# Optimization experiments

Measured on AMD Instinct MI355X. Metric: run time of the kernel, lower is better.

Reference implementation:

```python
import jax, jax.numpy as jnp
import numpy as np

TAU = 1.0  # gumbel-softmax temperature (self.temperature)


def setup_inputs() -> dict:
    key = jax.random.key(0)
    k1, k2, k3 = jax.random.split(key, 3)
    B, N, D = 4, 1024, 64
    node_features = jax.random.normal(k1, (B, N, D), dtype=jnp.float32)
    # edge_predictor params: Linear(2D -> D), Linear(D -> 1); stored as [in, out]
    W1 = jax.random.normal(k2, (2 * D, D), dtype=jnp.float32) * (1.0 / np.sqrt(2 * D))
    b1 = jnp.zeros((D,), dtype=jnp.float32)
    W2 = jax.random.normal(k3, (D, 1), dtype=jnp.float32) * (1.0 / np.sqrt(D))
    b2 = jnp.zeros((1,), dtype=jnp.float32)
    return {"node_features": node_features, "W1": W1, "b1": b1, "W2": W2, "b2": b2}


def reference(node_features, W1, b1, W2, b2):
    B, N, D = node_features.shape
    # cat([f_i, f_j]) @ W1 == f_i @ W1[:D] + f_j @ W1[D:] -> avoid [B,N,N,2D] concat
    h_src = jnp.einsum('bnd,de->bne', node_features, W1[:D])  # [B,N,D]
    h_dst = jnp.einsum('bnd,de->bne', node_features, W1[D:])  # [B,N,D]
    hidden = jax.nn.relu(h_src[:, :, None, :] + h_dst[:, None, :, :] + b1)  # [B,N,N,D]
    edge_logits = jnp.einsum('bijd,do->bij', hidden, W2) + b2[0]  # [B,N,N]
    edge_logits = 0.5 * (edge_logits + jnp.swapaxes(edge_logits, 1, 2))
    # training branch: gumbel-softmax (hard, straight-through) over [logit, 0] pair
    paired = jnp.stack([edge_logits, jnp.zeros_like(edge_logits)], axis=-1)  # [B,N,N,2]
    g = jax.random.gumbel(jax.random.key(42), paired.shape, dtype=paired.dtype)
    y_soft = jax.nn.softmax((paired + g) / TAU, axis=-1)
    hard = jax.nn.one_hot(jnp.argmax(y_soft, axis=-1), 2, dtype=y_soft.dtype)
    y = hard + y_soft - jax.lax.stop_gradient(y_soft)  # straight-through
    adj = y[..., 0] * (1.0 - jnp.eye(N, dtype=y.dtype))
    return adj, edge_logits
```

## Files before the change

kernel.cpp:

```cpp
#include <hip/hip_runtime.h>
#include <stdint.h>
#include <math.h>

#define NB 4
#define NN 1024
#define ND 64
#define RP 68

__device__ double g_hs64[NB * NN * ND];
__device__ double g_hd64[NB * NN * ND];
__device__ float  g_hs32[NB * NN * ND];
__device__ float  g_hd32[NB * NN * ND];
__device__ double g_w2d[ND];
__device__ float  g_w2f[ND];

__device__ __forceinline__ void threefry_core(uint32_t K0, uint32_t K1,
                                              uint32_t x0, uint32_t x1,
                                              uint32_t& o0, uint32_t& o1) {
  const uint32_t K2 = K0 ^ K1 ^ 0x1BD11BDAu;
  x0 += K0; x1 += K1;
#define TF_RND(r) { x0 += x1; x1 = (x1 << r) | (x1 >> (32 - r)); x1 ^= x0; }
  TF_RND(13) TF_RND(15) TF_RND(26) TF_RND(6)
  x0 += K1; x1 += K2 + 1u;
  TF_RND(17) TF_RND(29) TF_RND(16) TF_RND(24)
  x0 += K2; x1 += K0 + 2u;
  TF_RND(13) TF_RND(15) TF_RND(26) TF_RND(6)
  x0 += K0; x1 += K1 + 3u;
  TF_RND(17) TF_RND(29) TF_RND(16) TF_RND(24)
  x0 += K1; x1 += K2 + 4u;
  TF_RND(13) TF_RND(15) TF_RND(26) TF_RND(6)
  x0 += K2; x1 += K0 + 5u;
#undef TF_RND
  o0 = x0; o1 = x1;
}

__device__ __forceinline__ uint32_t rand_word(uint32_t L) {
  uint32_t o0, o1;
  threefry_core(0u, 42u, 0u, L, o0, o1);
  return o0 ^ o1;
}

__device__ __forceinline__ float u_from_word(uint32_t w) {
  uint32_t fb = (w >> 9) | 0x3f800000u;
  float f = __uint_as_float(fb) - 1.0f;
  const float tinyf = 1.17549435e-38f;
  return fmaxf(tinyf, f + tinyf);
}

__device__ __attribute__((noinline)) float decide_fallback(int b, int i, int j,
                                                           uint32_t m, double b2d) {
  const double* hsi = g_hs64 + ((size_t)(b * NN + i)) * ND;
  const double* hdi = g_hd64 + ((size_t)(b * NN + i)) * ND;
  const double* hsj = g_hs64 + ((size_t)(b * NN + j)) * ND;
  const double* hdj = g_hd64 + ((size_t)(b * NN + j)) * ND;
  double l1 = 0.0, l2 = 0.0;
  for (int d = 0; d < ND; ++d) {
    double w = g_w2d[d];
    l1 += fmax(hsi[d] + hdj[d], 0.0) * w;
    l2 += fmax(hsj[d] + hdi[d], 0.0) * w;
  }
  double sym = 0.5 * (l1 + l2) + b2d;
  double E = exp(sym);
  double L0 = -log((double)u_from_word(rand_word(2u * m)));
  double L1 = -log((double)u_from_word(rand_word(2u * m + 1u)));
  return (E * L1 >= L0) ? 1.0f : 0.0f;
}

__global__ __launch_bounds__(256) void stage1(const float* __restrict__ nf,
                                              const float* __restrict__ W1,
                                              const float* __restrict__ b1,
                                              const float* __restrict__ W2) {
  __shared__ float w1s[2 * ND][ND];
  __shared__ float rows[4][ND];
  const int tid = threadIdx.x;
  const float4* W14 = (const float4*)W1;
  float4* w1s4 = (float4*)w1s;
  #pragma unroll
  for (int p = 0; p < 8; ++p) w1s4[tid + 256 * p] = W14[tid + 256 * p];
  const int r = tid >> 6, e = tid & 63;
  const int bn = blockIdx.x * 4 + r;
  rows[r][e] = nf[bn * ND + e];
  __syncthreads();
  double accs = 0.0, accd = 0.0;
  #pragma unroll
  for (int k = 0; k < ND; ++k) {
    double x = (double)rows[r][k];
    accs = fma(x, (double)w1s[k][e], accs);
    accd = fma(x, (double)w1s[ND + k][e], accd);
  }
  accd += (double)b1[e];
  const int o = bn * ND + e;
  g_hs64[o] = accs;  g_hd64[o] = accd;
  g_hs32[o] = (float)accs;  g_hd32[o] = (float)accd;
  if (blockIdx.x == 0 && tid < ND) {
    g_w2d[tid] = (double)W2[tid];
    g_w2f[tid] = W2[tid];
  }
}

__global__ __launch_bounds__(256, 4) void stage2(const float* __restrict__ b2,
                                                 float* __restrict__ adj,
                                                 float* __restrict__ logits) {
  const int t = blockIdx.x;
  const int b = t / 528;
  const int k = t - b * 528;
#define TRI_S(x) ((x) * 32 - ((x) * ((x) - 1)) / 2)
  int bi = (int)((65.0 - sqrt((double)(4225 - 8 * k))) * 0.5);
  while (k >= TRI_S(bi + 1)) ++bi;
  while (k < TRI_S(bi)) --bi;
  const int bj = bi + (k - TRI_S(bi));
#undef TRI_S
  const int i0 = bi * 32, j0 = bj * 32;

  __shared__ float sh_si[32][RP], sh_di[32][RP];
  __shared__ float sh_sj[32][RP], sh_dj[32][RP];
  __shared__ float w2s[ND];

  const int tid = threadIdx.x;
  {
    const float4* src_si = (const float4*)(g_hs32 + ((size_t)(b * NN + i0)) * ND);
    const float4* src_di = (const float4*)(g_hd32 + ((size_t)(b * NN + i0)) * ND);
    const float4* src_sj = (const float4*)(g_hs32 + ((size_t)(b * NN + j0)) * ND);
    const float4* src_dj = (const float4*)(g_hd32 + ((size_t)(b * NN + j0)) * ND);
    #pragma unroll
    for (int p = 0; p < 2; ++p) {
      const int q = tid + 256 * p;
      const int r = q >> 4, c4 = (q & 15) << 2;
      *(float4*)&sh_si[r][c4] = src_si[q];
      *(float4*)&sh_di[r][c4] = src_di[q];
      *(float4*)&sh_sj[r][c4] = src_sj[q];
      *(float4*)&sh_dj[r][c4] = src_dj[q];
    }
    if (tid < ND) w2s[tid] = g_w2f[tid];
  }
  __syncthreads();

  const int tx = tid & 15, ty = tid >> 4;

  float a1[2][2] = {{0.f, 0.f}, {0.f, 0.f}};
  float a2[2][2] = {{0.f, 0.f}, {0.f, 0.f}};

  #pragma unroll 4
  for (int d = 0; d < ND; d += 4) {
    float wv[4], si[2][4], di[2][4], sj[2][4], dj[2][4];
    *(float4*)wv    = *(const float4*)&w2s[d];
    *(float4*)si[0] = *(const float4*)&sh_si[ty][d];
    *(float4*)si[1] = *(const float4*)&sh_si[ty + 16][d];
    *(float4*)di[0] = *(const float4*)&sh_di[ty][d];
    *(float4*)di[1] = *(const float4*)&sh_di[ty + 16][d];
    *(float4*)sj[0] = *(const float4*)&sh_sj[tx][d];
    *(float4*)sj[1] = *(const float4*)&sh_sj[tx + 16][d];
    *(float4*)dj[0] = *(const float4*)&sh_dj[tx][d];
    *(float4*)dj[1] = *(const float4*)&sh_dj[tx + 16][d];
    #pragma unroll
    for (int dd = 0; dd < 4; ++dd) {
      const float w = wv[dd];
      #pragma unroll
      for (int a = 0; a < 2; ++a)
        #pragma unroll
        for (int c = 0; c < 2; ++c) {
          a1[a][c] = fmaf(fmaxf(si[a][dd] + dj[c][dd], 0.f), w, a1[a][c]);
          a2[a][c] = fmaf(fmaxf(sj[c][dd] + di[a][dd], 0.f), w, a2[a][c]);
        }
    }
  }

  const float b2f = b2[0];
  const double b2d = (double)b2f;

  #pragma unroll
  for (int a = 0; a < 2; ++a)
    #pragma unroll
    for (int c = 0; c < 2; ++c) {
      const int i = i0 + ty + 16 * a;
      const int j = j0 + tx + 16 * c;
      const float symf = 0.5f * (a1[a][c] + a2[a][c]) + b2f;
      const uint32_t m1 = (uint32_t)((b * NN + i) * NN + j);
      const uint32_t m2 = (uint32_t)((b * NN + j) * NN + i);

      const float E = __expf(symf);
      const float L0a = -__logf(u_from_word(rand_word(2u * m1)));
      const float L1a = -__logf(u_from_word(rand_word(2u * m1 + 1u)));
      const float L0b = -__logf(u_from_word(rand_word(2u * m2)));
      const float L1b = -__logf(u_from_word(rand_word(2u * m2 + 1u)));

      float adj1, adj2;
      if (i == j) {
        adj1 = 0.f; adj2 = 0.f;
      } else {
        const float pa = E * L1a, da = pa - L0a;
        const float pb = E * L1b, db = pb - L0b;
        const bool flagA = (fabsf(da) < 2e-3f * (pa + L0a)) || ((pa + L0a) < 2e-6f);
        const bool flagB = (fabsf(db) < 2e-3f * (pb + L0b)) || ((pb + L0b) < 2e-6f);
        adj1 = flagA ? decide_fallback(b, i, j, m1, b2d) : (da >= 0.f ? 1.f : 0.f);
        adj2 = flagB ? decide_fallback(b, i, j, m2, b2d) : (db >= 0.f ? 1.f : 0.f);
      }

      logits[m1] = symf;
      logits[m2] = symf;
      adj[m1] = adj1;
      adj[m2] = adj2;
    }
}

extern "C" void kernel_launch(void* const* d_in, const int* in_sizes, int n_in,
                              void* d_out, int out_size, void* d_ws, size_t ws_size,
                              hipStream_t stream) {
  const float* nf = (const float*)d_in[0];
  const float* W1 = (const float*)d_in[1];
  const float* b1 = (const float*)d_in[2];
  const float* W2 = (const float*)d_in[3];
  const float* b2 = (const float*)d_in[4];

  float* adj    = (float*)d_out;
  float* logits = adj + (size_t)NB * NN * NN;

  stage1<<<dim3(NB * NN / 4), dim3(256), 0, stream>>>(nf, W1, b1, W2);
  stage2<<<dim3(NB * 528), dim3(256), 0, stream>>>(b2, adj, logits);
}
```

Measured before the change: 158.8 us.

## Use packed f32 math, halve shared tiles, raise occupancy in stage2

Stage2 now stages the node-feature tiles in two 32-column halves, which cuts shared memory per block roughly in half, and raises launch bounds from 4 to 8 blocks per SIMD. The inner loop uses inline-asm v_pk_add_f32 and v_pk_fma_f32 on pairs of channels, with two partial accumulators per output that are summed at the end. The goal is higher occupancy and fewer VALU instructions for the pairwise ReLU-dot compute. In exchange it adds an extra barrier and reload phase, the per-element fmax still breaks the packing, and the reordered float summation may shift values slightly near the fallback thresholds.

```diff
diff --git a/kernel.cpp b/kernel.cpp
--- a/kernel.cpp
+++ b/kernel.cpp
@@ -5,7 +5,20 @@
 #define NB 4
 #define NN 1024
 #define ND 64
-#define RP 68
+#define RPH 36
+
+typedef float v2f __attribute__((ext_vector_type(2)));
+
+__device__ __forceinline__ v2f pk_add(v2f a, v2f b) {
+  v2f d;
+  asm("v_pk_add_f32 %0, %1, %2" : "=v"(d) : "v"(a), "v"(b));
+  return d;
+}
+__device__ __forceinline__ v2f pk_fma(v2f a, v2f b, v2f c) {
+  v2f d;
+  asm("v_pk_fma_f32 %0, %1, %2, %3" : "=v"(d) : "v"(a), "v"(b), "v"(c));
+  return d;
+}
 
 __device__ double g_hs64[NB * NN * ND];
 __device__ double g_hd64[NB * NN * ND];
@@ -98,7 +111,7 @@
   }
 }
 
-__global__ __launch_bounds__(256, 4) void stage2(const float* __restrict__ b2,
+__global__ __launch_bounds__(256, 8) void stage2(const float* __restrict__ b2,
                                                  float* __restrict__ adj,
                                                  float* __restrict__ logits) {
   const int t = blockIdx.x;
@@ -112,56 +125,75 @@
 #undef TRI_S
   const int i0 = bi * 32, j0 = bj * 32;
 
-  __shared__ float sh_si[32][RP], sh_di[32][RP];
-  __shared__ float sh_sj[32][RP], sh_dj[32][RP];
+  __shared__ float sh[4][32][RPH];
   __shared__ float w2s[ND];
 
   const int tid = threadIdx.x;
-  {
-    const float4* src_si = (const float4*)(g_hs32 + ((size_t)(b * NN + i0)) * ND);
-    const float4* src_di = (const float4*)(g_hd32 + ((size_t)(b * NN + i0)) * ND);
-    const float4* src_sj = (const float4*)(g_hs32 + ((size_t)(b * NN + j0)) * ND);
-    const float4* src_dj = (const float4*)(g_hd32 + ((size_t)(b * NN + j0)) * ND);
-    #pragma unroll
-    for (int p = 0; p < 2; ++p) {
-      const int q = tid + 256 * p;
-      const int r = q >> 4, c4 = (q & 15) << 2;
-      *(float4*)&sh_si[r][c4] = src_si[q];
-      *(float4*)&sh_di[r][c4] = src_di[q];
-      *(float4*)&sh_sj[r][c4] = src_sj[q];
-      *(float4*)&sh_dj[r][c4] = src_dj[q];
+  const int tx = tid & 15, ty = tid >> 4;
+  if (tid < ND) w2s[tid] = g_w2f[tid];
+
+  v2f a1[2][2], a2[2][2];
+  #pragma unroll
+  for (int a = 0; a < 2; ++a)
+    #pragma unroll
+    for (int c = 0; c < 2; ++c) { a1[a][c] = (v2f)(0.f); a2[a][c] = (v2f)(0.f); }
+
+  const int srow = tid >> 3;
+  const int scol = (tid & 7) << 2;
+
+  #pragma unroll
+  for (int h = 0; h < 2; ++h) {
+    if (h) __syncthreads();
+    const int d0 = h * 32;
+    #pragma unroll
+    for (int p = 0; p < 4; ++p) {
+      const float* src = (p & 1) ? g_hd32 : g_hs32;
+      const int base = (p < 2) ? i0 : j0;
+      float4 v = *(const float4*)(src + ((size_t)(b * NN + base + srow)) * ND + d0 + scol);
+      *(float4*)&sh[p][srow][scol] = v;
     }
-    if (tid < ND) w2s[tid] = g_w2f[tid];
-  }
-  __syncthreads();
-
-  const int tx = tid & 15, ty = tid >> 4;
-
-  float a1[2][2] = {{0.f, 0.f}, {0.f, 0.f}};
-  float a2[2][2] = {{0.f, 0.f}, {0.f, 0.f}};
-
-  #pragma unroll 4
-  for (int d = 0; d < ND; d += 4) {
-    float wv[4], si[2][4], di[2][4], sj[2][4], dj[2][4];
-    *(float4*)wv    = *(const float4*)&w2s[d];
-    *(float4*)si[0] = *(const float4*)&sh_si[ty][d];
-    *(float4*)si[1] = *(const float4*)&sh_si[ty + 16][d];
-    *(float4*)di[0] = *(const float4*)&sh_di[ty][d];
-    *(float4*)di[1] = *(const float4*)&sh_di[ty + 16][d];
-    *(float4*)sj[0] = *(const float4*)&sh_sj[tx][d];
-    *(float4*)sj[1] = *(const float4*)&sh_sj[tx + 16][d];
-    *(float4*)dj[0] = *(const float4*)&sh_dj[tx][d];
-    *(float4*)dj[1] = *(const float4*)&sh_dj[tx + 16][d];
-    #pragma unroll
-    for (int dd = 0; dd < 4; ++dd) {
-      const float w = wv[dd];
+    __syncthreads();
+
+    #pragma unroll
+    for (int dd = 0; dd < 32; dd += 4) {
+      const float4 w4  = *(const float4*)&w2s[d0 + dd];
+      const float4 si0 = *(const float4*)&sh[0][ty][dd];
+      const float4 si1 = *(const float4*)&sh[0][ty + 16][dd];
+      const float4 di0 = *(const float4*)&sh[1][ty][dd];
+      const float4 di1 = *(const float4*)&sh[1][ty + 16][dd];
+      const float4 sj0 = *(const float4*)&sh[2][tx][dd];
+      const float4 sj1 = *(const float4*)&sh[2][tx + 16][dd];
+      const float4 dj0 = *(const float4*)&sh[3][tx][dd];
+      const float4 dj1 = *(const float4*)&sh[3][tx + 16][dd];
+
       #pragma unroll
-      for (int a = 0; a < 2; ++a)
+      for (int k2 = 0; k2 < 2; ++k2) {
+        v2f w_, si[2], di[2], sj[2], dj[2];
+        if (k2 == 0) {
+          w_ = (v2f){w4.x, w4.y};
+          si[0] = (v2f){si0.x, si0.y}; si[1] = (v2f){si1.x, si1.y};
+          di[0] = (v2f){di0.x, di0.y}; di[1] = (v2f){di1.x, di1.y};
+          sj[0] = (v2f){sj0.x, sj0.y}; sj[1] = (v2f){sj1.x, sj1.y};
+          dj[0] = (v2f){dj0.x, dj0.y}; dj[1] = (v2f){dj1.x, dj1.y};
+        } else {
+          w_ = (v2f){w4.z, w4.w};
+          si[0] = (v2f){si0.z, si0.w}; si[1] = (v2f){si1.z, si1.w};
+          di[0] = (v2f){di0.z, di0.w}; di[1] = (v2f){di1.z, di1.w};
+          sj[0] = (v2f){sj0.z, sj0.w}; sj[1] = (v2f){sj1.z, sj1.w};
+          dj[0] = (v2f){dj0.z, dj0.w}; dj[1] = (v2f){dj1.z, dj1.w};
+        }
         #pragma unroll
-        for (int c = 0; c < 2; ++c) {
-          a1[a][c] = fmaf(fmaxf(si[a][dd] + dj[c][dd], 0.f), w, a1[a][c]);
-          a2[a][c] = fmaf(fmaxf(sj[c][dd] + di[a][dd], 0.f), w, a2[a][c]);
-        }
+        for (int a = 0; a < 2; ++a)
+          #pragma unroll
+          for (int c = 0; c < 2; ++c) {
+            v2f t1 = pk_add(si[a], dj[c]);
+            t1.x = fmaxf(t1.x, 0.f); t1.y = fmaxf(t1.y, 0.f);
+            a1[a][c] = pk_fma(t1, w_, a1[a][c]);
+            v2f t2 = pk_add(sj[c], di[a]);
+            t2.x = fmaxf(t2.x, 0.f); t2.y = fmaxf(t2.y, 0.f);
+            a2[a][c] = pk_fma(t2, w_, a2[a][c]);
+          }
+      }
     }
   }
 
@@ -174,7 +206,9 @@
     for (int c = 0; c < 2; ++c) {
       const int i = i0 + ty + 16 * a;
       const int j = j0 + tx + 16 * c;
-      const float symf = 0.5f * (a1[a][c] + a2[a][c]) + b2f;
+      const float l1 = a1[a][c].x + a1[a][c].y;
+      const float l2 = a2[a][c].x + a2[a][c].y;
+      const float symf = 0.5f * (l1 + l2) + b2f;
       const uint32_t m1 = (uint32_t)((b * NN + i) * NN + j);
       const uint32_t m2 = (uint32_t)((b * NN + j) * NN + i);
 
```

Result: slower. 171.9 us (+8.3%).

## Stage output tiles through shared memory for coalesced float4 stores and halve LDS

Applied to the files above, without the earlier changes.

Stage2 now writes logits and both adjacency tiles into shared memory, then writes them out as coalesced float4 rows for both the (i,j) and transposed (j,i) blocks. Before, each thread did scattered scalar stores, and the transposed writes had a stride of NN. The feature tiles are loaded in two 32-wide halves, which halves shared-memory use, and launch bounds go up to 8 blocks per CU for higher occupancy. RNG work is also skipped on diagonal elements. In exchange there are extra __syncthreads barriers, and the transposed reads from shared memory may hit bank conflicts.

```diff
diff --git a/kernel.cpp b/kernel.cpp
--- a/kernel.cpp
+++ b/kernel.cpp
@@ -5,7 +5,8 @@
 #define NB 4
 #define NN 1024
 #define ND 64
-#define RP 68
+#define RPH 36
+#define TS 36
 
 __device__ double g_hs64[NB * NN * ND];
 __device__ double g_hd64[NB * NN * ND];
@@ -98,7 +99,7 @@
   }
 }
 
-__global__ __launch_bounds__(256, 4) void stage2(const float* __restrict__ b2,
+__global__ __launch_bounds__(256, 8) void stage2(const float* __restrict__ b2,
                                                  float* __restrict__ adj,
                                                  float* __restrict__ logits) {
   const int t = blockIdx.x;
@@ -112,82 +113,95 @@
 #undef TRI_S
   const int i0 = bi * 32, j0 = bj * 32;
 
-  __shared__ float sh_si[32][RP], sh_di[32][RP];
-  __shared__ float sh_sj[32][RP], sh_dj[32][RP];
+  __shared__ float sh[4 * 32 * RPH];
   __shared__ float w2s[ND];
 
   const int tid = threadIdx.x;
-  {
-    const float4* src_si = (const float4*)(g_hs32 + ((size_t)(b * NN + i0)) * ND);
-    const float4* src_di = (const float4*)(g_hd32 + ((size_t)(b * NN + i0)) * ND);
-    const float4* src_sj = (const float4*)(g_hs32 + ((size_t)(b * NN + j0)) * ND);
-    const float4* src_dj = (const float4*)(g_hd32 + ((size_t)(b * NN + j0)) * ND);
-    #pragma unroll
-    for (int p = 0; p < 2; ++p) {
-      const int q = tid + 256 * p;
-      const int r = q >> 4, c4 = (q & 15) << 2;
-      *(float4*)&sh_si[r][c4] = src_si[q];
-      *(float4*)&sh_di[r][c4] = src_di[q];
-      *(float4*)&sh_sj[r][c4] = src_sj[q];
-      *(float4*)&sh_dj[r][c4] = src_dj[q];
-    }
-    if (tid < ND) w2s[tid] = g_w2f[tid];
-  }
-  __syncthreads();
-
   const int tx = tid & 15, ty = tid >> 4;
+  if (tid < ND) w2s[tid] = g_w2f[tid];
 
   float a1[2][2] = {{0.f, 0.f}, {0.f, 0.f}};
   float a2[2][2] = {{0.f, 0.f}, {0.f, 0.f}};
 
-  #pragma unroll 4
-  for (int d = 0; d < ND; d += 4) {
-    float wv[4], si[2][4], di[2][4], sj[2][4], dj[2][4];
-    *(float4*)wv    = *(const float4*)&w2s[d];
-    *(float4*)si[0] = *(const float4*)&sh_si[ty][d];
-    *(float4*)si[1] = *(const float4*)&sh_si[ty + 16][d];
-    *(float4*)di[0] = *(const float4*)&sh_di[ty][d];
-    *(float4*)di[1] = *(const float4*)&sh_di[ty + 16][d];
-    *(float4*)sj[0] = *(const float4*)&sh_sj[tx][d];
-    *(float4*)sj[1] = *(const float4*)&sh_sj[tx + 16][d];
-    *(float4*)dj[0] = *(const float4*)&sh_dj[tx][d];
-    *(float4*)dj[1] = *(const float4*)&sh_dj[tx + 16][d];
+  const int srow = tid >> 3;
+  const int scol = (tid & 7) << 2;
+
+#define SH(p, r, c) sh[((p) * 32 + (r)) * RPH + (c)]
+
+  #pragma unroll
+  for (int h = 0; h < 2; ++h) {
+    if (h) __syncthreads();
+    const int d0 = h * 32;
     #pragma unroll
-    for (int dd = 0; dd < 4; ++dd) {
-      const float w = wv[dd];
+    for (int p = 0; p < 4; ++p) {
+      const float* src = (p & 1) ? g_hd32 : g_hs32;
+      const int base = (p < 2) ? i0 : j0;
+      float4 v = *(const float4*)(src + ((size_t)(b * NN + base + srow)) * ND + d0 + scol);
+      *(float4*)&SH(p, srow, scol) = v;
+    }
+    __syncthreads();
+
+    #pragma unroll
+    for (int dd = 0; dd < 32; dd += 4) {
+      const float4 w4  = *(const float4*)&w2s[d0 + dd];
+      const float4 si0 = *(const float4*)&SH(0, ty, dd);
+      const float4 si1 = *(const float4*)&SH(0, ty + 16, dd);
+      const float4 di0 = *(const float4*)&SH(1, ty, dd);
+      const float4 di1 = *(const float4*)&SH(1, ty + 16, dd);
+      const float4 sj0 = *(const float4*)&SH(2, tx, dd);
+      const float4 sj1 = *(const float4*)&SH(2, tx + 16, dd);
+      const float4 dj0 = *(const float4*)&SH(3, tx, dd);
+      const float4 dj1 = *(const float4*)&SH(3, tx + 16, dd);
+
+      const float* wv = (const float*)&w4;
+      const float* siA[2] = {(const float*)&si0, (const float*)&si1};
+      const float* diA[2] = {(const float*)&di0, (const float*)&di1};
+      const float* sjA[2] = {(const float*)&sj0, (const float*)&sj1};
+      const float* djA[2] = {(const float*)&dj0, (const float*)&dj1};
+
       #pragma unroll
-      for (int a = 0; a < 2; ++a)
+      for (int kk = 0; kk < 4; ++kk) {
+        const float w = wv[kk];
         #pragma unroll
-        for (int c = 0; c < 2; ++c) {
-          a1[a][c] = fmaf(fmaxf(si[a][dd] + dj[c][dd], 0.f), w, a1[a][c]);
-          a2[a][c] = fmaf(fmaxf(sj[c][dd] + di[a][dd], 0.f), w, a2[a][c]);
-        }
+        for (int a = 0; a < 2; ++a)
+          #pragma unroll
+          for (int c = 0; c < 2; ++c) {
+            a1[a][c] = fmaf(fmaxf(siA[a][kk] + djA[c][kk], 0.f), w, a1[a][c]);
+            a2[a][c] = fmaf(fmaxf(sjA[c][kk] + diA[a][kk], 0.f), w, a2[a][c]);
+          }
+      }
     }
   }
 
   const float b2f = b2[0];
   const double b2d = (double)b2f;
+
+  float* Lg = sh;
+  float* A1 = sh + 32 * TS;
+  float* A2 = sh + 64 * TS;
+
+  __syncthreads();
 
   #pragma unroll
   for (int a = 0; a < 2; ++a)
     #pragma unroll
     for (int c = 0; c < 2; ++c) {
-      const int i = i0 + ty + 16 * a;
-      const int j = j0 + tx + 16 * c;
+      const int rr = ty + 16 * a;
+      const int cc = tx + 16 * c;
+      const int i = i0 + rr, j = j0 + cc;
       const float symf = 0.5f * (a1[a][c] + a2[a][c]) + b2f;
       const uint32_t m1 = (uint32_t)((b * NN + i) * NN + j);
       const uint32_t m2 = (uint32_t)((b * NN + j) * NN + i);
-
-      const float E = __expf(symf);
-      const float L0a = -__logf(u_from_word(rand_word(2u * m1)));
-      const float L1a = -__logf(u_from_word(rand_word(2u * m1 + 1u)));
-      const float L0b = -__logf(u_from_word(rand_word(2u * m2)));
-      const float L1b = -__logf(u_from_word(rand_word(2u * m2 + 1u)));
 
       float adj1, adj2;
       if (i == j) {
         adj1 = 0.f; adj2 = 0.f;
       } else {
+        const float E = __expf(symf);
+        const float L0a = -__logf(u_from_word(rand_word(2u * m1)));
+        const float L1a = -__logf(u_from_word(rand_word(2u * m1 + 1u)));
+        const float L0b = -__logf(u_from_word(rand_word(2u * m2)));
+        const float L1b = -__logf(u_from_word(rand_word(2u * m2 + 1u)));
         const float pa = E * L1a, da = pa - L0a;
         const float pb = E * L1b, db = pb - L0b;
         const bool flagA = (fabsf(da) < 2e-3f * (pa + L0a)) || ((pa + L0a) < 2e-6f);
@@ -196,11 +210,30 @@
         adj2 = flagB ? decide_fallback(b, i, j, m2, b2d) : (db >= 0.f ? 1.f : 0.f);
       }
 
-      logits[m1] = symf;
-      logits[m2] = symf;
-      adj[m1] = adj1;
-      adj[m2] = adj2;
+      Lg[rr * TS + cc] = symf;
+      A1[rr * TS + cc] = adj1;
+      A2[cc * TS + rr] = adj2;
     }
+
+  __syncthreads();
+
+  {
+    const int r = tid >> 3;
+    const int c4 = (tid & 7) << 2;
+    const size_t rowI = ((size_t)(b * NN + i0 + r)) * NN + j0 + c4;
+    const size_t rowJ = ((size_t)(b * NN + j0 + r)) * NN + i0 + c4;
+
+    *(float4*)&logits[rowI] = *(const float4*)&Lg[r * TS + c4];
+    float4 lt;
+    lt.x = Lg[(c4 + 0) * TS + r];
+    lt.y = Lg[(c4 + 1) * TS + r];
+    lt.z = Lg[(c4 + 2) * TS + r];
+    lt.w = Lg[(c4 + 3) * TS + r];
+    *(float4*)&logits[rowJ] = lt;
+    *(float4*)&adj[rowI] = *(const float4*)&A1[r * TS + c4];
+    *(float4*)&adj[rowJ] = *(const float4*)&A2[r * TS + c4];
+  }
+#undef SH
 }
 
 extern "C" void kernel_launch(void* const* d_in, const int* in_sizes, int n_in,
```

Measured after the change: 171.1 us. +7.7%, slower.

## Defer ambiguous gumbel decisions to a separate exact-recompute kernel via atomic queue

Applied to the files above, without the earlier changes.

The double-precision fallback for near-tie edges is no longer called inline in the main tile kernel. Flagged indices are appended to a workspace queue with an atomic counter, and a third kernel recomputes them exactly. This removes divergent, register-heavy fallback code from the hot loop, and the RNG/exp work is also moved inside the i!=j branch. In exchange it adds a memset, an extra kernel launch and atomics. If the workspace capacity is too small, overflowing entries silently keep the float decision.

```diff
diff --git a/kernel.cpp b/kernel.cpp
--- a/kernel.cpp
+++ b/kernel.cpp
@@ -47,8 +47,7 @@
   return fmaxf(tinyf, f + tinyf);
 }
 
-__device__ __attribute__((noinline)) float decide_fallback(int b, int i, int j,
-                                                           uint32_t m, double b2d) {
+__device__ float decide_exact(int b, int i, int j, uint32_t m, double b2d) {
   const double* hsi = g_hs64 + ((size_t)(b * NN + i)) * ND;
   const double* hdi = g_hd64 + ((size_t)(b * NN + i)) * ND;
   const double* hsj = g_hs64 + ((size_t)(b * NN + j)) * ND;
@@ -100,7 +99,9 @@
 
 __global__ __launch_bounds__(256, 4) void stage2(const float* __restrict__ b2,
                                                  float* __restrict__ adj,
-                                                 float* __restrict__ logits) {
+                                                 float* __restrict__ logits,
+                                                 uint32_t* __restrict__ flags,
+                                                 uint32_t cap) {
   const int t = blockIdx.x;
   const int b = t / 528;
   const int k = t - b * 528;
@@ -166,7 +167,6 @@
   }
 
   const float b2f = b2[0];
-  const double b2d = (double)b2f;
 
   #pragma unroll
   for (int a = 0; a < 2; ++a)
@@ -178,22 +178,29 @@
       const uint32_t m1 = (uint32_t)((b * NN + i) * NN + j);
       const uint32_t m2 = (uint32_t)((b * NN + j) * NN + i);
 
-      const float E = __expf(symf);
-      const float L0a = -__logf(u_from_word(rand_word(2u * m1)));
-      const float L1a = -__logf(u_from_word(rand_word(2u * m1 + 1u)));
-      const float L0b = -__logf(u_from_word(rand_word(2u * m2)));
-      const float L1b = -__logf(u_from_word(rand_word(2u * m2 + 1u)));
-
       float adj1, adj2;
       if (i == j) {
         adj1 = 0.f; adj2 = 0.f;
       } else {
+        const float E = __expf(symf);
+        const float L0a = -__logf(u_from_word(rand_word(2u * m1)));
+        const float L1a = -__logf(u_from_word(rand_word(2u * m1 + 1u)));
+        const float L0b = -__logf(u_from_word(rand_word(2u * m2)));
+        const float L1b = -__logf(u_from_word(rand_word(2u * m2 + 1u)));
         const float pa = E * L1a, da = pa - L0a;
         const float pb = E * L1b, db = pb - L0b;
+        adj1 = (da >= 0.f) ? 1.f : 0.f;
+        adj2 = (db >= 0.f) ? 1.f : 0.f;
         const bool flagA = (fabsf(da) < 2e-3f * (pa + L0a)) || ((pa + L0a) < 2e-6f);
         const bool flagB = (fabsf(db) < 2e-3f * (pb + L0b)) || ((pb + L0b) < 2e-6f);
-        adj1 = flagA ? decide_fallback(b, i, j, m1, b2d) : (da >= 0.f ? 1.f : 0.f);
-        adj2 = flagB ? decide_fallback(b, i, j, m2, b2d) : (db >= 0.f ? 1.f : 0.f);
+        if (flagA) {
+          uint32_t slot = atomicAdd(flags, 1u);
+          if (slot < cap) flags[4 + slot] = m1;
+        }
+        if (flagB) {
+          uint32_t slot = atomicAdd(flags, 1u);
+          if (slot < cap) flags[4 + slot] = m2;
+        }
       }
 
       logits[m1] = symf;
@@ -201,6 +208,22 @@
       adj[m1] = adj1;
       adj[m2] = adj2;
     }
+}
+
+__global__ __launch_bounds__(256) void stage3(const float* __restrict__ b2,
+                                              float* __restrict__ adj,
+                                              const uint32_t* __restrict__ flags,
+                                              uint32_t cap) {
+  const uint32_t n = min(flags[0], cap);
+  const double b2d = (double)b2[0];
+  for (uint32_t idx = blockIdx.x * 256 + threadIdx.x; idx < n;
+       idx += gridDim.x * 256) {
+    const uint32_t m = flags[4 + idx];
+    const int b = (int)(m >> 20);
+    const int i = (int)((m >> 10) & 1023);
+    const int j = (int)(m & 1023);
+    adj[m] = decide_exact(b, i, j, m, b2d);
+  }
 }
 
 extern "C" void kernel_launch(void* const* d_in, const int* in_sizes, int n_in,
@@ -215,6 +238,15 @@
   float* adj    = (float*)d_out;
   float* logits = adj + (size_t)NB * NN * NN;
 
+  uint32_t* flags = (uint32_t*)d_ws;
+  uint32_t cap = 0;
+  if (ws_size >= 64) {
+    size_t c = (ws_size - 16) / 4;
+    cap = (c > 4194304u) ? 4194304u : (uint32_t)c;
+  }
+
+  hipMemsetAsync(d_ws, 0, 16, stream);
   stage1<<<dim3(NB * NN / 4), dim3(256), 0, stream>>>(nf, W1, b1, W2);
-  stage2<<<dim3(NB * 528), dim3(256), 0, stream>>>(b2, adj, logits);
-}
+  stage2<<<dim3(NB * 528), dim3(256), 0, stream>>>(b2, adj, logits, flags, cap);
+  stage3<<<dim3(128), dim3(256), 0, stream>>>(b2, adj, flags, cap);
+}
```

Measured after the change: 201.6 us. 26.9% more time.
